# Kernel optimization log

Hardware: AMD Instinct MI355X
Metric: run time of the kernel (lower is better)

## Reference

```python
import jax, jax.numpy as jnp
import numpy as np

NUM_HEADS = 16
KEY_DIM = 64
D_MODEL = NUM_HEADS * KEY_DIM
BATCH = 2
SEQ = 2048


def _rope_tables(seq_len, dim, dtype):
    # matches RotaryPositionalEmbedding: inv_freq = exp(arange(0,dim,2) * (-ln(10000)/dim))
    pos = jnp.arange(seq_len, dtype=dtype)                      # [S]
    inv_freq = jnp.exp(jnp.arange(0, dim, 2, dtype=dtype) * (-np.log(10000.0) / dim))  # [D/2]
    angles = pos[:, None] * inv_freq[None, :]                   # [S, D/2]
    return jnp.sin(angles), jnp.cos(angles)


def _apply_rope(x, sin, cos):
    # x: [B, S, H, D]; sin/cos: [S, D/2] broadcast over batch and heads
    sin = sin[None, :, None, :]
    cos = cos[None, :, None, :]
    x1, x2 = jnp.split(x, 2, axis=-1)
    return jnp.concatenate([cos * x1 - sin * x2, sin * x1 + cos * x2], axis=-1)


def setup_inputs() -> dict:
    key = jax.random.key(0)
    ks = jax.random.split(key, 5)
    s = 1.0 / np.sqrt(D_MODEL)
    return {
        "inputs": jax.random.normal(ks[0], (BATCH, SEQ, D_MODEL), jnp.float32),
        "Wq": jax.random.normal(ks[1], (D_MODEL, D_MODEL), jnp.float32) * s,
        "bq": jnp.zeros((D_MODEL,), jnp.float32),
        "Wk": jax.random.normal(ks[2], (D_MODEL, D_MODEL), jnp.float32) * s,
        "bk": jnp.zeros((D_MODEL,), jnp.float32),
        "Wv": jax.random.normal(ks[3], (D_MODEL, D_MODEL), jnp.float32) * s,
        "bv": jnp.zeros((D_MODEL,), jnp.float32),
        "Wo": jax.random.normal(ks[4], (D_MODEL, D_MODEL), jnp.float32) * s,
        "bo": jnp.zeros((D_MODEL,), jnp.float32),
    }


def reference(inputs, Wq, bq, Wk, bk, Wv, bv, Wo, bo):
    B, S, _ = inputs.shape
    # QKV projections, split into heads: [B, S, H, Dk]
    q = (inputs @ Wq + bq).reshape(B, S, NUM_HEADS, KEY_DIM)
    k = (inputs @ Wk + bk).reshape(B, S, NUM_HEADS, KEY_DIM)
    v = (inputs @ Wv + bv).reshape(B, S, NUM_HEADS, KEY_DIM)
    # rotary embedding on q/k (per-head dim = KEY_DIM)
    sin, cos = _rope_tables(S, KEY_DIM, inputs.dtype)
    q = _apply_rope(q, sin, cos)
    k = _apply_rope(k, sin, cos)
    # attention: [B, H, S, S]
    scores = jnp.einsum("bshd,bthd->bhst", q, k) / jnp.sqrt(
        jnp.asarray(KEY_DIM, inputs.dtype))
    weights = jax.nn.softmax(scores, axis=-1)  # dropout inactive (training=False)
    ctx = jnp.einsum("bhst,bthd->bshd", weights, v).reshape(B, S, D_MODEL)
    return ctx @ Wo + bo
```

## Files before the change

### kernel.cpp

```cpp
#include <hip/hip_runtime.h>
#include <math.h>

#define NH 16
#define KD 64
#define DMODEL 1024
#define BATCH 2
#define SEQ 2048
#define MROWS (BATCH*SEQ)

typedef float f32x4 __attribute__((ext_vector_type(4)));
typedef float f32x16 __attribute__((ext_vector_type(16)));
typedef __bf16 bf16x8 __attribute__((ext_vector_type(8)));

__device__ __forceinline__ unsigned short f2bf(float x) {
    union { float f; unsigned u; } a; a.f = x;
    unsigned r = a.u + 0x7fffu + ((a.u >> 16) & 1u);
    return (unsigned short)(r >> 16);
}
__device__ __forceinline__ unsigned cvt_pk_bf16(float lo, float hi) {
    unsigned r;
    asm("v_cvt_pk_bf16_f32 %0, %1, %2" : "=v"(r) : "v"(lo), "v"(hi));
    return r;
}
__device__ __forceinline__ float exp2_hw(float x) {
    float r;
    asm("v_exp_f32 %0, %1" : "=v"(r) : "v"(x));
    return r;
}

__device__ __forceinline__ void gl2lds16(const void* gsrc, void* ldst) {
    __builtin_amdgcn_global_load_lds(
        (const __attribute__((address_space(1))) void*)gsrc,
        (__attribute__((address_space(3))) void*)ldst, 16, 0, 0);
}

__global__ __launch_bounds__(256) void k_prep(const float* __restrict__ x,
                                              const float* __restrict__ W0,
                                              const float* __restrict__ W1,
                                              const float* __restrict__ W2,
                                              const float* __restrict__ W3,
                                              float* __restrict__ sin_t,
                                              float* __restrict__ cos_t,
                                              unsigned short* __restrict__ xh,
                                              unsigned short* __restrict__ Th) {
    __shared__ float L[64][65];
    const int bid = blockIdx.x;
    const int tid = threadIdx.x;
    if (bid < 256) {
        int idx = bid * 256 + tid;
        int s = idx >> 5, i = idx & 31;
        float invf = expf((float)(2 * i) * (-logf(10000.0f) / (float)KD));
        float ang = (float)s * invf;
        sin_t[idx] = sinf(ang);
        cos_t[idx] = cosf(ang);
        return;
    }
    if (bid < 4352) {
        int idx = (bid - 256) * 256 + tid;
        float4 v = reinterpret_cast<const float4*>(x)[idx];
        ushort4 h;
        h.x = f2bf(v.x); h.y = f2bf(v.y); h.z = f2bf(v.z); h.w = f2bf(v.w);
        reinterpret_cast<ushort4*>(xh)[idx] = h;
        return;
    }
    int r = bid - 4352;
    int z = r >> 8;
    int rr = r & 255;
    const int n0 = (rr & 15) * 64, k0 = (rr >> 4) * 64;
    const float* W = (z == 0) ? W0 : (z == 1) ? W1 : (z == 2) ? W2 : W3;
    const size_t zoff = (size_t)z * DMODEL * DMODEL;
#pragma unroll
    for (int it = 0; it < 4; ++it) {
        int idx = tid + it * 256;
        int rw = idx >> 4;
        int c4 = (idx & 15) * 4;
        float4 v = *reinterpret_cast<const float4*>(&W[(size_t)(k0 + rw) * DMODEL + n0 + c4]);
        L[rw][c4 + 0] = v.x; L[rw][c4 + 1] = v.y; L[rw][c4 + 2] = v.z; L[rw][c4 + 3] = v.w;
    }
    __syncthreads();
    int rn = tid >> 2;
    int ks = (tid & 3) * 16;
#pragma unroll
    for (int g = 0; g < 4; ++g) {
        ushort4 h;
        h.x = f2bf(L[ks + g * 4 + 0][rn]);
        h.y = f2bf(L[ks + g * 4 + 1][rn]);
        h.z = f2bf(L[ks + g * 4 + 2][rn]);
        h.w = f2bf(L[ks + g * 4 + 3][rn]);
        size_t o = zoff + (size_t)(n0 + rn) * DMODEL + k0 + ks + g * 4;
        *reinterpret_cast<ushort4*>(&Th[o]) = h;
    }
}

__global__ __launch_bounds__(256) void k_mgemm_qkv(const unsigned short* __restrict__ Ah_g,
                                                   const unsigned short* __restrict__ Wp,
                                                   const float* __restrict__ bq,
                                                   const float* __restrict__ bk,
                                                   const float* __restrict__ bv,
                                                   unsigned short* __restrict__ qh_,
                                                   unsigned short* __restrict__ kh_,
                                                   unsigned short* __restrict__ vth,
                                                   const float* __restrict__ sin_t,
                                                   const float* __restrict__ cos_t) {
    __shared__ unsigned short Ah[2][128 * 64];
    __shared__ unsigned short Bh[2][3][64 * 64];
    const int tid = threadIdx.x;
    const int lane = tid & 63;
    const int w = tid >> 6;

    int bid = blockIdx.x;
    int wg = (bid & 7) * 64 + (bid >> 3);
    const int m0 = (wg >> 4) * 128;
    const int n0 = (wg & 15) * 64;
    const size_t WE = (size_t)DMODEL * DMODEL;

    size_t a_goff[4]; int a_ldst[4];
#pragma unroll
    for (int it = 0; it < 4; ++it) {
        int off = it * 4096 + w * 1024 + lane * 16;
        int row = off >> 7;
        int pg = (off >> 4) & 7;
        int lg = pg ^ (row & 7);
        a_goff[it] = (size_t)(m0 + row) * DMODEL + lg * 8;
        a_ldst[it] = it * 2048 + w * 512;
    }
    size_t b_goff[2]; int b_ldst[2];
#pragma unroll
    for (int it = 0; it < 2; ++it) {
        int off = it * 4096 + w * 1024 + lane * 16;
        int row = off >> 7;
        int pg = (off >> 4) & 7;
        int lg = pg ^ (row & 7);
        b_goff[it] = (size_t)(n0 + row) * DMODEL + lg * 8;
        b_ldst[it] = it * 2048 + w * 512;
    }

    int aoff[2][2], boff[4][2];
#pragma unroll
    for (int mf = 0; mf < 2; ++mf)
#pragma unroll
        for (int ks = 0; ks < 2; ++ks) {
            int row = w * 32 + mf * 16 + (lane & 15);
            int g = ks * 4 + (lane >> 4);
            aoff[mf][ks] = row * 64 + ((g ^ (row & 7)) * 8);
        }
#pragma unroll
    for (int nf = 0; nf < 4; ++nf)
#pragma unroll
        for (int ks = 0; ks < 2; ++ks) {
            int row = nf * 16 + (lane & 15);
            int g = ks * 4 + (lane >> 4);
            boff[nf][ks] = row * 64 + ((g ^ (row & 7)) * 8);
        }

    f32x4 acc[3][2][4];
#pragma unroll
    for (int z = 0; z < 3; ++z)
#pragma unroll
        for (int mf = 0; mf < 2; ++mf)
#pragma unroll
            for (int nf = 0; nf < 4; ++nf) acc[z][mf][nf] = (f32x4){0.f, 0.f, 0.f, 0.f};

#define STAGEG(BUF, KT) do {                                                  \
        int k0_ = (KT) * 64;                                                  \
        gl2lds16(Ah_g + a_goff[0] + k0_, &Ah[BUF][a_ldst[0]]);                \
        gl2lds16(Ah_g + a_goff[1] + k0_, &Ah[BUF][a_ldst[1]]);                \
        gl2lds16(Ah_g + a_goff[2] + k0_, &Ah[BUF][a_ldst[2]]);                \
        gl2lds16(Ah_g + a_goff[3] + k0_, &Ah[BUF][a_ldst[3]]);                \
        gl2lds16(Wp + 0 * WE + b_goff[0] + k0_, &Bh[BUF][0][b_ldst[0]]);      \
        gl2lds16(Wp + 0 * WE + b_goff[1] + k0_, &Bh[BUF][0][b_ldst[1]]);      \
        gl2lds16(Wp + 1 * WE + b_goff[0] + k0_, &Bh[BUF][1][b_ldst[0]]);      \
        gl2lds16(Wp + 1 * WE + b_goff[1] + k0_, &Bh[BUF][1][b_ldst[1]]);      \
        gl2lds16(Wp + 2 * WE + b_goff[0] + k0_, &Bh[BUF][2][b_ldst[0]]);      \
        gl2lds16(Wp + 2 * WE + b_goff[1] + k0_, &Bh[BUF][2][b_ldst[1]]);      \
    } while (0)

    STAGEG(0, 0);

    for (int kt = 0; kt < 16; ++kt) {
        const int cur = kt & 1;
        asm volatile("s_waitcnt vmcnt(0)" ::: "memory");
        __builtin_amdgcn_s_barrier();
        if (kt < 15) STAGEG(cur ^ 1, kt + 1);
#pragma unroll
        for (int ks = 0; ks < 2; ++ks) {
            bf16x8 ah[2];
#pragma unroll
            for (int mf = 0; mf < 2; ++mf)
                ah[mf] = *reinterpret_cast<const bf16x8*>(&Ah[cur][aoff[mf][ks]]);
#pragma unroll
            for (int z = 0; z < 3; ++z) {
                bf16x8 bh[4];
#pragma unroll
                for (int nf = 0; nf < 4; ++nf)
                    bh[nf] = *reinterpret_cast<const bf16x8*>(&Bh[cur][z][boff[nf][ks]]);
#pragma unroll
                for (int mf = 0; mf < 2; ++mf)
#pragma unroll
                    for (int nf = 0; nf < 4; ++nf)
                        acc[z][mf][nf] = __builtin_amdgcn_mfma_f32_16x16x32_bf16(ah[mf], bh[nf], acc[z][mf][nf], 0, 0, 0);
            }
        }
    }
#undef STAGEG

    const int c = lane & 15;
    const int rq = lane >> 4;
    float bvq[4], bvk[4], bvv[4];
#pragma unroll
    for (int nf = 0; nf < 4; ++nf) {
        bvq[nf] = bq[n0 + nf * 16 + c];
        bvk[nf] = bk[n0 + nf * 16 + c];
        bvv[nf] = bv[n0 + nf * 16 + c];
    }

#pragma unroll
    for (int mf = 0; mf < 2; ++mf) {
        int mbase = m0 + w * 32 + mf * 16 + rq * 4;
#pragma unroll
        for (int z = 0; z < 2; ++z) {
            const float* bb_ = (z == 0) ? bvq : bvk;
            unsigned short* Ohi = (z == 0) ? qh_ : kh_;
#pragma unroll
            for (int r2 = 0; r2 < 4; ++r2) {
                int m = mbase + r2;
                int srow = m & (SEQ - 1);
                float x0 = acc[z][mf][0][r2] + bb_[0];
                float x1 = acc[z][mf][1][r2] + bb_[1];
                float x2 = acc[z][mf][2][r2] + bb_[2];
                float x3 = acc[z][mf][3][r2] + bb_[3];
                float s0 = sin_t[srow * 32 + c],      c0 = cos_t[srow * 32 + c];
                float s1 = sin_t[srow * 32 + 16 + c], c1 = cos_t[srow * 32 + 16 + c];
                float o0 = c0 * x0 - s0 * x2;
                float o2 = s0 * x0 + c0 * x2;
                float o1 = c1 * x1 - s1 * x3;
                float o3 = s1 * x1 + c1 * x3;
                if (z == 0) {
                    const float qs = 0.18033688011112042f;
                    o0 *= qs; o1 *= qs; o2 *= qs; o3 *= qs;
                }
                float ov[4] = { o0, o1, o2, o3 };
                size_t base = (size_t)m * DMODEL + n0 + c;
#pragma unroll
                for (int nf = 0; nf < 4; ++nf)
                    Ohi[base + nf * 16] = f2bf(ov[nf]);
            }
        }
        {
            int bb = mbase >> 11;
            int s = mbase & (SEQ - 1);
            int h = n0 >> 6;
#pragma unroll
            for (int nf = 0; nf < 4; ++nf) {
                ushort4 h4;
                float v0 = acc[2][mf][nf][0] + bvv[nf];
                float v1 = acc[2][mf][nf][1] + bvv[nf];
                float v2 = acc[2][mf][nf][2] + bvv[nf];
                float v3 = acc[2][mf][nf][3] + bvv[nf];
                h4.x = f2bf(v0); h4.y = f2bf(v1); h4.z = f2bf(v2); h4.w = f2bf(v3);
                int d = nf * 16 + c;
                size_t o = ((size_t)((bb * NH + h) * KD + d)) * SEQ + s;
                *reinterpret_cast<ushort4*>(&vth[o]) = h4;
            }
        }
    }
}

__global__ __launch_bounds__(256) void k_mgemm_o(const unsigned short* __restrict__ Ah_g,
                                                 const unsigned short* __restrict__ Bh_g,
                                                 const float* __restrict__ bias,
                                                 float* __restrict__ Cf) {
    __shared__ unsigned short Ah[2][128 * 64];
    __shared__ unsigned short Bh[2][64 * 64];
    const int tid = threadIdx.x;
    const int lane = tid & 63;
    const int w = tid >> 6;

    int bid = blockIdx.x;
    int wg = (bid & 7) * 64 + (bid >> 3);
    const int m0 = (wg >> 4) * 128;
    const int n0 = (wg & 15) * 64;

    size_t a_goff[4]; int a_ldst[4];
#pragma unroll
    for (int it = 0; it < 4; ++it) {
        int off = it * 4096 + w * 1024 + lane * 16;
        int row = off >> 7;
        int pg = (off >> 4) & 7;
        int lg = pg ^ (row & 7);
        a_goff[it] = (size_t)(m0 + row) * DMODEL + lg * 8;
        a_ldst[it] = it * 2048 + w * 512;
    }
    size_t b_goff[2]; int b_ldst[2];
#pragma unroll
    for (int it = 0; it < 2; ++it) {
        int off = it * 4096 + w * 1024 + lane * 16;
        int row = off >> 7;
        int pg = (off >> 4) & 7;
        int lg = pg ^ (row & 7);
        b_goff[it] = (size_t)(n0 + row) * DMODEL + lg * 8;
        b_ldst[it] = it * 2048 + w * 512;
    }

    int aoff[2][2], boff[4][2];
#pragma unroll
    for (int mf = 0; mf < 2; ++mf)
#pragma unroll
        for (int ks = 0; ks < 2; ++ks) {
            int row = w * 32 + mf * 16 + (lane & 15);
            int g = ks * 4 + (lane >> 4);
            aoff[mf][ks] = row * 64 + ((g ^ (row & 7)) * 8);
        }
#pragma unroll
    for (int nf = 0; nf < 4; ++nf)
#pragma unroll
        for (int ks = 0; ks < 2; ++ks) {
            int row = nf * 16 + (lane & 15);
            int g = ks * 4 + (lane >> 4);
            boff[nf][ks] = row * 64 + ((g ^ (row & 7)) * 8);
        }

    f32x4 acc[2][4];
#pragma unroll
    for (int mf = 0; mf < 2; ++mf)
#pragma unroll
        for (int nf = 0; nf < 4; ++nf) acc[mf][nf] = (f32x4){0.f, 0.f, 0.f, 0.f};

#define STAGEG(BUF, KT) do {                                                  \
        int k0_ = (KT) * 64;                                                  \
        gl2lds16(Ah_g + a_goff[0] + k0_, &Ah[BUF][a_ldst[0]]);                \
        gl2lds16(Ah_g + a_goff[1] + k0_, &Ah[BUF][a_ldst[1]]);                \
        gl2lds16(Ah_g + a_goff[2] + k0_, &Ah[BUF][a_ldst[2]]);                \
        gl2lds16(Ah_g + a_goff[3] + k0_, &Ah[BUF][a_ldst[3]]);                \
        gl2lds16(Bh_g + b_goff[0] + k0_, &Bh[BUF][b_ldst[0]]);                \
        gl2lds16(Bh_g + b_goff[1] + k0_, &Bh[BUF][b_ldst[1]]);                \
    } while (0)

    STAGEG(0, 0);

    for (int kt = 0; kt < 16; ++kt) {
        const int cur = kt & 1;
        asm volatile("s_waitcnt vmcnt(0)" ::: "memory");
        __builtin_amdgcn_s_barrier();
        if (kt < 15) STAGEG(cur ^ 1, kt + 1);
#pragma unroll
        for (int ks = 0; ks < 2; ++ks) {
            bf16x8 ah[2], bh[4];
#pragma unroll
            for (int mf = 0; mf < 2; ++mf)
                ah[mf] = *reinterpret_cast<const bf16x8*>(&Ah[cur][aoff[mf][ks]]);
#pragma unroll
            for (int nf = 0; nf < 4; ++nf)
                bh[nf] = *reinterpret_cast<const bf16x8*>(&Bh[cur][boff[nf][ks]]);
#pragma unroll
            for (int mf = 0; mf < 2; ++mf)
#pragma unroll
                for (int nf = 0; nf < 4; ++nf)
                    acc[mf][nf] = __builtin_amdgcn_mfma_f32_16x16x32_bf16(ah[mf], bh[nf], acc[mf][nf], 0, 0, 0);
        }
    }
#undef STAGEG

    const int c = lane & 15;
    const int rq = lane >> 4;
    float bv[4];
#pragma unroll
    for (int nf = 0; nf < 4; ++nf) bv[nf] = bias[n0 + nf * 16 + c];
#pragma unroll
    for (int mf = 0; mf < 2; ++mf) {
        int mbase = m0 + w * 32 + mf * 16 + rq * 4;
#pragma unroll
        for (int nf = 0; nf < 4; ++nf)
#pragma unroll
            for (int r = 0; r < 4; ++r)
                Cf[(size_t)(mbase + r) * DMODEL + n0 + nf * 16 + c] = acc[mf][nf][r] + bv[nf];
    }
}

__global__ __launch_bounds__(256) void k_attn(const unsigned short* __restrict__ qhi,
                                              const unsigned short* __restrict__ khi,
                                              const unsigned short* __restrict__ vthi,
                                              unsigned short* __restrict__ ch) {
    __shared__ unsigned short Kh[2][64 * 64];
    __shared__ unsigned short Vh[3][64 * 64];

    const int tid  = threadIdx.x;
    const int lane = tid & 63;
    const int w    = tid >> 6;

    int bid = blockIdx.x;
    int wg  = (bid & 7) * 64 + (bid >> 3);
    const int qt = wg & 15;
    const int h  = (wg >> 4) & 15;
    const int b  = wg >> 8;
    const int q0 = qt * 128;

    const int l31 = lane & 31;
    const int lh  = lane >> 5;

    bf16x8 qf[4];
#pragma unroll
    for (int ks = 0; ks < 4; ++ks) {
        int row = q0 + w * 32 + l31;
        qf[ks] = *reinterpret_cast<const bf16x8*>(
            qhi + ((size_t)(b * SEQ + row) * NH + h) * KD + ks * 16 + lh * 8);
    }

    size_t gK[2], gV[2]; int ld_[2];
#pragma unroll
    for (int it = 0; it < 2; ++it) {
        int off = it * 4096 + tid * 16;
        int row = off >> 7;
        int pg = (off >> 4) & 7;
        int lg = pg ^ (row & 7);
        gK[it] = ((size_t)(b * SEQ + row) * NH + h) * KD + lg * 8;
        gV[it] = ((size_t)(b * NH + h) * KD + row) * SEQ + lg * 8;
        ld_[it] = it * 2048 + w * 512;
    }

    int foff[2][4];
#pragma unroll
    for (int tb = 0; tb < 2; ++tb)
#pragma unroll
        for (int ks = 0; ks < 4; ++ks)
            foff[tb][ks] = (tb * 32 + l31) * 64 + (((ks * 2 + lh) ^ (lane & 7)) * 8);

    f32x16 acc[2];
#pragma unroll
    for (int db = 0; db < 2; ++db)
#pragma unroll
        for (int r = 0; r < 16; ++r) acc[db][r] = 0.f;
    float l_part = 0.f;

    unsigned paw[4][4];
    union U8 { unsigned u[4]; bf16x8 v; };

#define STAGE(KB, VB, TT) do {                                               \
        size_t kadv = (size_t)(TT) * 64 * NH * KD;                           \
        size_t vadv = (size_t)(TT) * 64;                                     \
        gl2lds16(khi  + gK[0] + kadv, &Kh[KB][ld_[0]]);                      \
        gl2lds16(khi  + gK[1] + kadv, &Kh[KB][ld_[1]]);                      \
        gl2lds16(vthi + gV[0] + vadv, &Vh[VB][ld_[0]]);                      \
        gl2lds16(vthi + gV[1] + vadv, &Vh[VB][ld_[1]]);                      \
    } while (0)

#define PV_STEP(VSRC) do {                                                   \
        _Pragma("unroll")                                                    \
        for (int db = 0; db < 2; ++db) {                                     \
            _Pragma("unroll")                                                \
            for (int ks = 0; ks < 4; ++ks) {                                 \
                bf16x8 vf = *reinterpret_cast<const bf16x8*>(&Vh[VSRC][foff[db][ks]]); \
                U8 pa; pa.u[0] = paw[ks][0]; pa.u[1] = paw[ks][1];           \
                pa.u[2] = paw[ks][2]; pa.u[3] = paw[ks][3];                  \
                acc[db] = __builtin_amdgcn_mfma_f32_32x32x16_bf16(pa.v, vf, acc[db], 0, 0, 0); \
            }                                                                \
        }                                                                    \
    } while (0)

    STAGE(0, 0, 0);

    int vnext = 1;
    int vprev = 2;

    for (int t = 0; t < 32; ++t) {
        const int ck = t & 1;
        asm volatile("s_waitcnt vmcnt(0)" ::: "memory");
        __builtin_amdgcn_s_barrier();
        if (t < 31) STAGE(ck ^ 1, vnext, t + 1);

        __builtin_amdgcn_s_setprio(1);
        f32x16 s[2];
#pragma unroll
        for (int tb = 0; tb < 2; ++tb) {
#pragma unroll
            for (int r = 0; r < 16; ++r) s[tb][r] = 0.f;
#pragma unroll
            for (int ks = 0; ks < 4; ++ks) {
                bf16x8 kf = *reinterpret_cast<const bf16x8*>(&Kh[ck][foff[tb][ks]]);
                s[tb] = __builtin_amdgcn_mfma_f32_32x32x16_bf16(kf, qf[ks], s[tb], 0, 0, 0);
            }
        }
        if (t > 0) PV_STEP(vprev);
        __builtin_amdgcn_s_setprio(0);

#pragma unroll
        for (int tb = 0; tb < 2; ++tb) {
            float e[16];
#pragma unroll
            for (int r = 0; r < 16; ++r) {
                e[r] = exp2_hw(s[tb][r]);
                l_part += e[r];
            }
#pragma unroll
            for (int half = 0; half < 2; ++half) {
                unsigned pk01 = cvt_pk_bf16(e[half * 8 + 0], e[half * 8 + 1]);
                unsigned pk23 = cvt_pk_bf16(e[half * 8 + 2], e[half * 8 + 3]);
                unsigned pk45 = cvt_pk_bf16(e[half * 8 + 4], e[half * 8 + 5]);
                unsigned pk67 = cvt_pk_bf16(e[half * 8 + 6], e[half * 8 + 7]);
                asm volatile("v_permlane32_swap_b32 %0, %1" : "+v"(pk01), "+v"(pk45));
                asm volatile("v_permlane32_swap_b32 %0, %1" : "+v"(pk23), "+v"(pk67));
                paw[tb * 2 + half][0] = pk01;
                paw[tb * 2 + half][1] = pk23;
                paw[tb * 2 + half][2] = pk45;
                paw[tb * 2 + half][3] = pk67;
            }
        }

        vnext = (vnext == 2) ? 0 : vnext + 1;
        vprev = (vprev == 2) ? 0 : vprev + 1;
    }

    PV_STEP(vprev);
#undef PV_STEP
#undef STAGE

    l_part += __shfl_xor(l_part, 32);
    float linv[16];
#pragma unroll
    for (int r = 0; r < 16; ++r) {
        int q = (r & 3) + 8 * (r >> 2) + 4 * lh;
        linv[r] = 1.0f / __shfl(l_part, q);
    }
#pragma unroll
    for (int db = 0; db < 2; ++db) {
#pragma unroll
        for (int r = 0; r < 16; ++r) {
            int q = (r & 3) + 8 * (r >> 2) + 4 * lh;
            int qg = q0 + w * 32 + q;
            int d = db * 32 + l31;
            ch[((size_t)(b * SEQ + qg) * NH + h) * KD + d] = f2bf(acc[db][r] * linv[r]);
        }
    }
}

extern "C" void kernel_launch(void* const* d_in, const int* in_sizes, int n_in,
                              void* d_out, int out_size, void* d_ws, size_t ws_size,
                              hipStream_t stream) {
    const float* x  = (const float*)d_in[0];
    const float* Wq = (const float*)d_in[1];
    const float* bq = (const float*)d_in[2];
    const float* Wk = (const float*)d_in[3];
    const float* bk = (const float*)d_in[4];
    const float* Wv = (const float*)d_in[5];
    const float* bv = (const float*)d_in[6];
    const float* Wo = (const float*)d_in[7];
    const float* bo = (const float*)d_in[8];
    float* out = (float*)d_out;

    const size_t NE = (size_t)MROWS * DMODEL;
    const size_t WE = (size_t)DMODEL * DMODEL;
    float* ws    = (float*)d_ws;
    float* sin_t = ws;
    float* cos_t = sin_t + SEQ * 32;
    unsigned short* p = (unsigned short*)(cos_t + SEQ * 32);
    unsigned short* xh   = p; p += NE;
    unsigned short* qh_  = p; p += NE;
    unsigned short* kh_  = p; p += NE;
    unsigned short* vth  = p; p += NE;
    unsigned short* wth  = p; p += 4 * WE;
    unsigned short* ctxh = xh;

    k_prep<<<5376, 256, 0, stream>>>(x, Wq, Wk, Wv, Wo, sin_t, cos_t, xh, wth);

    k_mgemm_qkv<<<512, 256, 0, stream>>>(xh, wth, bq, bk, bv, qh_, kh_, vth, sin_t, cos_t);

    k_attn<<<512, 256, 0, stream>>>(qh_, kh_, vth, ctxh);

    k_mgemm_o<<<512, 256, 0, stream>>>(ctxh, wth + 3 * WE, bo, out);
}
```

Measured before the change: 111.3 us.

## Split attention KV range in two and combine partials in a separate kernel

Attention work is split along the key dimension into two halves, doubling the number of workgroups from 512 to 1024 to fill more compute units. Each half writes unnormalized fp32 partial accumulators and row sums to workspace, and a new combine kernel adds them, normalizes, and converts to bf16. This relies on the softmax having no running max (exp2 of raw scores), so partials can simply be summed. In exchange it adds a kernel launch and about 32 MB of extra fp32 traffic.

Result: slower. 123.4 us (+10.9%).

```diff
diff --git a/kernel.cpp b/kernel.cpp
--- a/kernel.cpp
+++ b/kernel.cpp
@@ -380,7 +380,8 @@
 __global__ __launch_bounds__(256) void k_attn(const unsigned short* __restrict__ qhi,
                                               const unsigned short* __restrict__ khi,
                                               const unsigned short* __restrict__ vthi,
-                                              unsigned short* __restrict__ ch) {
+                                              float* __restrict__ accf,
+                                              float* __restrict__ lsum) {
     __shared__ unsigned short Kh[2][64 * 64];
     __shared__ unsigned short Vh[3][64 * 64];
 
@@ -389,11 +390,13 @@
     const int w    = tid >> 6;
 
     int bid = blockIdx.x;
-    int wg  = (bid & 7) * 64 + (bid >> 3);
+    int wg  = (bid & 7) * 128 + (bid >> 3);
     const int qt = wg & 15;
     const int h  = (wg >> 4) & 15;
-    const int b  = wg >> 8;
+    const int b  = (wg >> 8) & 1;
+    const int sp = wg >> 9;
     const int q0 = qt * 128;
+    const int t_begin = sp * 16;
 
     const int l31 = lane & 31;
     const int lh  = lane >> 5;
@@ -457,16 +460,17 @@
         }                                                                    \
     } while (0)
 
-    STAGE(0, 0, 0);
+    STAGE(0, 0, t_begin);
 
     int vnext = 1;
     int vprev = 2;
 
-    for (int t = 0; t < 32; ++t) {
-        const int ck = t & 1;
+    for (int ti = 0; ti < 16; ++ti) {
+        const int t = t_begin + ti;
+        const int ck = ti & 1;
         asm volatile("s_waitcnt vmcnt(0)" ::: "memory");
         __builtin_amdgcn_s_barrier();
-        if (t < 31) STAGE(ck ^ 1, vnext, t + 1);
+        if (ti < 15) STAGE(ck ^ 1, vnext, t + 1);
 
         __builtin_amdgcn_s_setprio(1);
         f32x16 s[2];
@@ -480,7 +484,7 @@
                 s[tb] = __builtin_amdgcn_mfma_f32_32x32x16_bf16(kf, qf[ks], s[tb], 0, 0, 0);
             }
         }
-        if (t > 0) PV_STEP(vprev);
+        if (ti > 0) PV_STEP(vprev);
         __builtin_amdgcn_s_setprio(0);
 
 #pragma unroll
@@ -515,11 +519,10 @@
 #undef STAGE
 
     l_part += __shfl_xor(l_part, 32);
-    float linv[16];
-#pragma unroll
-    for (int r = 0; r < 16; ++r) {
-        int q = (r & 3) + 8 * (r >> 2) + 4 * lh;
-        linv[r] = 1.0f / __shfl(l_part, q);
+    float* accp = accf + (size_t)sp * MROWS * DMODEL;
+    if (lh == 0) {
+        int qg = q0 + w * 32 + l31;
+        lsum[(size_t)sp * (MROWS * NH) + (size_t)(b * SEQ + qg) * NH + h] = l_part;
     }
 #pragma unroll
     for (int db = 0; db < 2; ++db) {
@@ -528,9 +531,35 @@
             int q = (r & 3) + 8 * (r >> 2) + 4 * lh;
             int qg = q0 + w * 32 + q;
             int d = db * 32 + l31;
-            ch[((size_t)(b * SEQ + qg) * NH + h) * KD + d] = f2bf(acc[db][r] * linv[r]);
-        }
-    }
+            accp[((size_t)(b * SEQ + qg) * NH + h) * KD + d] = acc[db][r];
+        }
+    }
+}
+
+__global__ __launch_bounds__(256) void k_comb(const float* __restrict__ accf,
+                                              const float* __restrict__ lsum,
+                                              unsigned short* __restrict__ ch) {
+    int idx = blockIdx.x * 256 + threadIdx.x;
+    size_t o = (size_t)idx * 8;
+    int rI = (int)(o >> 6);
+    float inv = 1.0f / (lsum[rI] + lsum[MROWS * NH + rI]);
+    const float* a0 = accf;
+    const float* a1 = accf + (size_t)MROWS * DMODEL;
+    float4 x0 = *reinterpret_cast<const float4*>(a0 + o);
+    float4 x1 = *reinterpret_cast<const float4*>(a0 + o + 4);
+    float4 y0 = *reinterpret_cast<const float4*>(a1 + o);
+    float4 y1 = *reinterpret_cast<const float4*>(a1 + o + 4);
+    ushort4 h0, h1;
+    h0.x = f2bf((x0.x + y0.x) * inv);
+    h0.y = f2bf((x0.y + y0.y) * inv);
+    h0.z = f2bf((x0.z + y0.z) * inv);
+    h0.w = f2bf((x0.w + y0.w) * inv);
+    h1.x = f2bf((x1.x + y1.x) * inv);
+    h1.y = f2bf((x1.y + y1.y) * inv);
+    h1.z = f2bf((x1.z + y1.z) * inv);
+    h1.w = f2bf((x1.w + y1.w) * inv);
+    *reinterpret_cast<ushort4*>(ch + o) = h0;
+    *reinterpret_cast<ushort4*>(ch + o + 4) = h1;
 }
 
 extern "C" void kernel_launch(void* const* d_in, const int* in_sizes, int n_in,
@@ -558,13 +587,17 @@
     unsigned short* kh_  = p; p += NE;
     unsigned short* vth  = p; p += NE;
     unsigned short* wth  = p; p += 4 * WE;
+    float* accf = (float*)p;
+    float* lsum = accf + 2 * NE;
     unsigned short* ctxh = xh;
 
     k_prep<<<5376, 256, 0, stream>>>(x, Wq, Wk, Wv, Wo, sin_t, cos_t, xh, wth);
 
     k_mgemm_qkv<<<512, 256, 0, stream>>>(xh, wth, bq, bk, bv, qh_, kh_, vth, sin_t, cos_t);
 
-    k_attn<<<512, 256, 0, stream>>>(qh_, kh_, vth, ctxh);
+    k_attn<<<1024, 256, 0, stream>>>(qh_, kh_, vth, accf, lsum);
+
+    k_comb<<<(int)(NE / 8 / 256), 256, 0, stream>>>(accf, lsum, ctxh);
 
     k_mgemm_o<<<512, 256, 0, stream>>>(ctxh, wth + 3 * WE, bo, out);
 }
```
